# Optimization experiments

Measured on AMD Instinct MI355X. Metric: run time of the kernel, lower is better.

Reference implementation:

```python
import jax, jax.numpy as jnp
import numpy as np

B, LW, LE, D, H = 16, 512, 128, 1024, 16
DH = D // H  # 64
L = LW + LE


def _heads(x):
    # [B, L, D] -> [B, H, L, DH]
    b, l, _ = x.shape
    return x.reshape(b, l, H, DH).transpose(0, 2, 1, 3)


def setup_inputs() -> dict:
    key = jax.random.key(0)
    ks = jax.random.split(key, 20)
    s = 0.02
    def w(k):
        return jax.random.normal(k, (D, D), dtype=jnp.float32) * s
    def b(k):
        return jax.random.normal(k, (D,), dtype=jnp.float32) * s
    return {
        "word_hidden_states": jax.random.normal(ks[0], (B, LW, D), dtype=jnp.float32),
        "entity_hidden_states": jax.random.normal(ks[1], (B, LE, D), dtype=jnp.float32),
        "attention_mask": jnp.zeros((B, 1, 1, L), dtype=jnp.float32),
        "layer_num": 0,
        "qw": w(ks[2]), "qb": b(ks[3]),
        "kw": w(ks[4]), "kb": b(ks[5]),
        "vw": w(ks[6]), "vb": b(ks[7]),
        "w2e_qw": w(ks[8]), "w2e_qb": b(ks[9]),
        "w2e_kw": w(ks[10]), "w2e_kb": b(ks[11]),
        "e2w_qw": w(ks[12]), "e2w_qb": b(ks[13]),
        "e2w_kw": w(ks[14]), "e2w_kb": b(ks[15]),
    }


def reference(word_hidden_states, entity_hidden_states, attention_mask, layer_num,
              qw, qb, kw, kb, vw, vb,
              w2e_qw, w2e_qb, w2e_kw, w2e_kb,
              e2w_qw, e2w_qb, e2w_kw, e2w_kb):
    h = jnp.concatenate([word_hidden_states, entity_hidden_states], axis=1)  # [B,L,D]
    q = _heads(h @ qw + qb)
    k = _heads(h @ kw + kb)
    v = _heads(h @ vw + vb)
    scores = jnp.einsum("bhqd,bhkd->bhqk", q, k)  # [B,H,L,L]

    # cross-block gate scores
    w2e_q = _heads(word_hidden_states @ w2e_qw + w2e_qb)    # [B,H,LW,DH]
    w2e_k = _heads(entity_hidden_states @ w2e_kw + w2e_kb)  # [B,H,LE,DH]
    w2e = jnp.einsum("bhqd,bhkd->bhqk", w2e_q, w2e_k)       # [B,H,LW,LE]
    e2w_q = _heads(entity_hidden_states @ e2w_qw + e2w_qb)  # [B,H,LE,DH]
    e2w_k = _heads(word_hidden_states @ e2w_kw + e2w_kb)    # [B,H,LW,DH]
    e2w = jnp.einsum("bhqd,bhkd->bhqk", e2w_q, e2w_k)       # [B,H,LE,LW]

    # masked_scatter fills only cross blocks; elsewhere gate raw score is 0,
    # so sigmoid(0)*-10 = -5 on the word-word and entity-entity blocks.
    gate = jnp.full(scores.shape, -5.0, dtype=scores.dtype)
    gate = gate.at[:, :, :LW, LW:].set(jax.nn.sigmoid(w2e) * -10.0)
    gate = gate.at[:, :, LW:, :LW].set(jax.nn.sigmoid(e2w) * -10.0)

    scores = (scores + gate) / np.sqrt(DH).astype(np.float32)
    scores = scores + attention_mask
    probs = jax.nn.softmax(scores, axis=-1)
    ctx = jnp.einsum("bhqk,bhkd->bhqd", probs, v)  # [B,H,L,DH]
    ctx = ctx.transpose(0, 2, 1, 3).reshape(h.shape[0], L, D)
    return ctx[:, :LW, :], ctx[:, LW:, :]
```

## Files before the change

### kernel.cpp

```cpp
#include <hip/hip_runtime.h>
#include <hip/hip_bf16.h>
#include <stdint.h>

#define B_   16
#define LW_  512
#define LE_  128
#define L_   640
#define D_   1024
#define H_   16
#define DH_  64
#define M_   (B_*L_)
#define N_   (7*D_)
#define K_   D_

typedef __attribute__((ext_vector_type(8))) short short8;
typedef __attribute__((ext_vector_type(4))) float float4v;

__device__ __forceinline__ unsigned short f2bf(float x){
    union { float f; uint32_t u; } v; v.f = x;
    uint32_t u = v.u;
    return (unsigned short)((u + 0x7FFFu + ((u >> 16) & 1u)) >> 16);
}

__global__ __launch_bounds__(256) void prep_h(const float* __restrict__ word,
                                              const float* __restrict__ ent,
                                              unsigned short* __restrict__ hb){
    int idx = blockIdx.x*256 + threadIdx.x;
    int row = idx >> 7;
    int c   = (idx & 127) << 3;
    int b = row / L_, l = row - b*L_;
    const float* src = (l < LW_) ? (word + ((size_t)b*LW_ + l)*D_ + c)
                                 : (ent  + ((size_t)b*LE_ + (l-LW_))*D_ + c);
    float4 a0 = ((const float4*)src)[0];
    float4 a1 = ((const float4*)src)[1];
    uint4 o;
    o.x = f2bf(a0.x) | ((uint32_t)f2bf(a0.y)<<16);
    o.y = f2bf(a0.z) | ((uint32_t)f2bf(a0.w)<<16);
    o.z = f2bf(a1.x) | ((uint32_t)f2bf(a1.y)<<16);
    o.w = f2bf(a1.z) | ((uint32_t)f2bf(a1.w)<<16);
    *(uint4*)(hb + (size_t)row*D_ + c) = o;
}

__global__ __launch_bounds__(256) void prep_w(const float* __restrict__ w0, const float* __restrict__ w1,
                                              const float* __restrict__ w2, const float* __restrict__ w3,
                                              const float* __restrict__ w4, const float* __restrict__ w5,
                                              const float* __restrict__ w6,
                                              unsigned short* __restrict__ bt){
    __shared__ float t[64][65];
    int id = blockIdx.x;
    int kt = id & 15;
    int ntile = id >> 4;
    int p = ntile >> 4;
    int nin = (ntile & 15) * 64;
    const float* wp = (p==0)?w0:(p==1)?w1:(p==2)?w2:(p==3)?w3:(p==4)?w4:(p==5)?w5:w6;
    int k0 = kt*64;
    int tr  = threadIdx.x >> 4;
    int tc4 = (threadIdx.x & 15) * 4;
    for (int pass = 0; pass < 4; ++pass){
        int kl = pass*16 + tr;
        const float4 v = *(const float4*)(wp + (size_t)(k0+kl)*D_ + nin + tc4);
        t[kl][tc4+0]=v.x; t[kl][tc4+1]=v.y; t[kl][tc4+2]=v.z; t[kl][tc4+3]=v.w;
    }
    __syncthreads();
    for (int pass = 0; pass < 4; ++pass){
        int nl = pass*16 + tr;
        uint2 pk;
        pk.x = f2bf(t[tc4+0][nl]) | ((uint32_t)f2bf(t[tc4+1][nl])<<16);
        pk.y = f2bf(t[tc4+2][nl]) | ((uint32_t)f2bf(t[tc4+3][nl])<<16);
        *(uint2*)(bt + (size_t)(ntile*64 + nl)*K_ + k0 + tc4) = pk;
    }
}

__global__ __launch_bounds__(256) void prep_bias(const float* __restrict__ b0, const float* __restrict__ b1,
                                                 const float* __restrict__ b2, const float* __restrict__ b3,
                                                 const float* __restrict__ b4, const float* __restrict__ b5,
                                                 const float* __restrict__ b6,
                                                 float* __restrict__ biasAll){
    int n = blockIdx.x*256 + threadIdx.x;
    int p = n >> 10, c = n & 1023;
    const float* bp = (p==0)?b0:(p==1)?b1:(p==2)?b2:(p==3)?b3:(p==4)?b4:(p==5)?b5:b6;
    biasAll[n] = bp[c];
}

__global__ __launch_bounds__(256, 4) void gemm_proj(const unsigned short* __restrict__ hb,
                                                    const unsigned short* __restrict__ bt,
                                                    const float* __restrict__ biasAll,
                                                    unsigned short* __restrict__ C,
                                                    unsigned short* __restrict__ Vt){
    __shared__ unsigned short sA[128*64];
    __shared__ unsigned short sB[128*64];
    int tid = threadIdx.x;
    int wave = tid >> 6, lane = tid & 63;
    int quad = lane >> 4, l16 = lane & 15;
    int bm = blockIdx.x % 80, bn = blockIdx.x / 80;
    int m0 = bm*128, n0 = bn*128;
    int wm = wave >> 1, wn = wave & 1;
    float4v acc[4][4] = {};

    for (int kk = 0; kk < K_; kk += 64) {
        #pragma unroll
        for (int i = 0; i < 4; ++i) {
            int idx = i*256 + tid;
            int row = idx >> 3;
            int c8  = (((idx & 7) ^ (row & 7)) << 3);
            const unsigned short* ga = hb + (size_t)(m0 + row)*K_ + kk + c8;
            __builtin_amdgcn_global_load_lds(
                (const __attribute__((address_space(1))) void*)ga,
                (__attribute__((address_space(3))) void*)(sA + ((i*256 + wave*64) << 3)), 16, 0, 0);
            const unsigned short* gb = bt + (size_t)(n0 + row)*K_ + kk + c8;
            __builtin_amdgcn_global_load_lds(
                (const __attribute__((address_space(1))) void*)gb,
                (__attribute__((address_space(3))) void*)(sB + ((i*256 + wave*64) << 3)), 16, 0, 0);
        }
        __syncthreads();
        #pragma unroll
        for (int s = 0; s < 2; ++s) {
            short8 af[4], bf[4];
            #pragma unroll
            for (int i=0;i<4;i++){
                int row = wm*64 + i*16 + l16;
                af[i] = *(const short8*)(sA + (row << 6) + (((s*4 + quad) ^ (row & 7)) << 3));
            }
            #pragma unroll
            for (int j=0;j<4;j++){
                int row = wn*64 + j*16 + l16;
                bf[j] = *(const short8*)(sB + (row << 6) + (((s*4 + quad) ^ (row & 7)) << 3));
            }
            #pragma unroll
            for (int i=0;i<4;i++)
                #pragma unroll
                for (int j=0;j<4;j++)
                    acc[i][j] = __builtin_amdgcn_mfma_f32_16x16x32_bf16(af[i], bf[j], acc[i][j], 0,0,0);
        }
        __syncthreads();
    }

    bool isV = (n0 >= 2*D_) && (n0 < 3*D_);
    #pragma unroll
    for (int i=0;i<4;i++){
        int mrow = m0 + wm*64 + i*16 + quad*4;
        #pragma unroll
        for (int j=0;j<4;j++){
            int ncol = n0 + wn*64 + j*16 + l16;
            float bias = biasAll[ncol];
            if (!isV) {
                #pragma unroll
                for (int r=0;r<4;r++)
                    C[(size_t)(mrow + r)*N_ + ncol] = f2bf(acc[i][j][r] + bias);
            } else {
                int nv = ncol - 2*D_;
                int hh = nv >> 6, dd = nv & 63;
                int bb = mrow / L_, ll = mrow - bb*L_;
                uint2 pk;
                pk.x = f2bf(acc[i][j][0]+bias) | ((uint32_t)f2bf(acc[i][j][1]+bias)<<16);
                pk.y = f2bf(acc[i][j][2]+bias) | ((uint32_t)f2bf(acc[i][j][3]+bias)<<16);
                *(uint2*)(Vt + ((size_t)(bb*H_ + hh)*DH_ + dd)*L_ + ll) = pk;
            }
        }
    }
}


__device__ __forceinline__ void tile_ld(const unsigned short* __restrict__ g, size_t stride,
                                        unsigned short* lds, int wave, int lane){
    #pragma unroll
    for (int p = 0; p < 2; ++p){
        int c = p*256 + wave*64 + lane;
        int r = c >> 3, js = c & 7;
        const unsigned short* ga = g + (size_t)r*stride + ((js ^ (r & 7)) << 3);
        __builtin_amdgcn_global_load_lds(
            (const __attribute__((address_space(1))) void*)ga,
            (__attribute__((address_space(3))) void*)(lds + ((p*256 + wave*64) << 3)), 16, 0, 0);
    }
}

__device__ __forceinline__ short8 frag64(const unsigned short* lds, int row, int jj){
    return *(const short8*)(lds + (row << 6) + (((jj ^ (row & 7)) << 3)));
}

__global__ __launch_bounds__(256, 2) void attn(const unsigned short* __restrict__ C,
                                               const unsigned short* __restrict__ Vt,
                                               const float* __restrict__ mask,
                                               float* __restrict__ out){
    int id = blockIdx.x;
    int qt = id % 5; id /= 5;
    int h  = id % H_; int b = id / H_;
    bool isWord = (qt < 4);
    int tid = threadIdx.x, wave = tid>>6, lane = tid&63, quad = lane>>4, l16 = lane&15;

    __shared__ unsigned short sK0 [64*64];
    __shared__ unsigned short sK1 [64*64];
    __shared__ unsigned short sGK0[64*64];
    __shared__ unsigned short sGK1[64*64];
    __shared__ unsigned short sV0 [64*64];
    __shared__ unsigned short sV1 [64*64];
    __shared__ unsigned short sP  [64*64];
    __shared__ float sMask[L_];

    const unsigned short* Kg  = C  + (size_t)(b*L_)*N_ + D_ + h*DH_;
    const unsigned short* GKg = C  + (size_t)(b*L_)*N_ + (isWord?4:6)*D_ + h*DH_;
    const unsigned short* Vg  = Vt + ((size_t)(b*H_ + h)*DH_)*L_;

    tile_ld(Kg, N_, sK0, wave, lane);
    tile_ld(Vg, L_, sV0, wave, lane);
    if (!isWord) tile_ld(GKg, N_, sGK0, wave, lane);

    for (int i = tid; i < L_; i += 256) sMask[i] = mask[b*L_ + i];

    int qrowbase = b*L_ + qt*128 + wave*32;
    short8 qf[2][2], gqf[2][2];
    #pragma unroll
    for (int mi=0; mi<2; ++mi){
        const unsigned short* qb_ = C + (size_t)(qrowbase + mi*16 + l16)*N_ + h*DH_;
        const unsigned short* gq_ = C + (size_t)(qrowbase + mi*16 + l16)*N_ + (isWord?3:5)*D_ + h*DH_;
        qf[mi][0]  = *(const short8*)(qb_ + quad*8);
        qf[mi][1]  = *(const short8*)(qb_ + 32 + quad*8);
        gqf[mi][0] = *(const short8*)(gq_ + quad*8);
        gqf[mi][1] = *(const short8*)(gq_ + 32 + quad*8);
    }

    float4v O[2][4] = {};
    float lrow[2][4] = {};

    __syncthreads();

    auto step = [&](int kt,
                    unsigned short* sKc, unsigned short* sGKc, unsigned short* sVc,
                    unsigned short* sKn, unsigned short* sGKn, unsigned short* sVn){
        if (kt < 9) {
            tile_ld(Kg + (size_t)((kt+1)*64)*N_, N_, sKn, wave, lane);
            tile_ld(Vg + (kt+1)*64, L_, sVn, wave, lane);
            bool g1 = isWord ? (kt+1 >= 8) : (kt+1 < 8);
            if (g1) tile_ld(GKg + (size_t)((kt+1)*64)*N_, N_, sGKn, wave, lane);
        }
        bool gated = isWord ? (kt >= 8) : (kt < 8);

        float4v S[2][4];
        #pragma unroll
        for (int nt=0; nt<4; ++nt){
            short8 k0 = frag64(sKc, nt*16 + l16, quad);
            short8 k1 = frag64(sKc, nt*16 + l16, 4 + quad);
            #pragma unroll
            for (int mi=0; mi<2; ++mi){
                float4v s = {};
                s = __builtin_amdgcn_mfma_f32_16x16x32_bf16(qf[mi][0], k0, s, 0,0,0);
                s = __builtin_amdgcn_mfma_f32_16x16x32_bf16(qf[mi][1], k1, s, 0,0,0);
                S[mi][nt] = s;
            }
        }
        if (gated) {
            #pragma unroll
            for (int nt=0; nt<4; ++nt){
                short8 g0 = frag64(sGKc, nt*16 + l16, quad);
                short8 g1 = frag64(sGKc, nt*16 + l16, 4 + quad);
                #pragma unroll
                for (int mi=0; mi<2; ++mi){
                    float4v g = {};
                    g = __builtin_amdgcn_mfma_f32_16x16x32_bf16(gqf[mi][0], g0, g, 0,0,0);
                    g = __builtin_amdgcn_mfma_f32_16x16x32_bf16(gqf[mi][1], g1, g, 0,0,0);
                    #pragma unroll
                    for (int r=0;r<4;r++){
                        float sig = 1.f/(1.f + __expf(-g[r]));
                        S[mi][nt][r] = 0.125f*S[mi][nt][r] - 1.25f*sig;
                    }
                }
            }
        } else {
            #pragma unroll
            for (int mi=0;mi<2;mi++)
                #pragma unroll
                for (int nt=0;nt<4;nt++)
                    #pragma unroll
                    for (int r=0;r<4;r++) S[mi][nt][r] = 0.125f*S[mi][nt][r] - 0.625f;
        }
        #pragma unroll
        for (int mi=0;mi<2;mi++){
            #pragma unroll
            for (int nt=0;nt<4;nt++){
                float mv = sMask[kt*64 + nt*16 + l16];
                #pragma unroll
                for (int r=0;r<4;r++){
                    float p = __expf(S[mi][nt][r] + mv);
                    S[mi][nt][r] = p;
                    lrow[mi][r] += p;
                }
            }
            #pragma unroll
            for (int nt=0;nt<4;nt++)
                #pragma unroll
                for (int r=0;r<4;r++){
                    int row = wave*16 + quad*4 + r;
                    int col = nt*16 + l16;
                    int j = col >> 3, jo = col & 7;
                    sP[(row<<6) + (((j ^ (row & 7))<<3) | jo)] = f2bf(S[mi][nt][r]);
                }
            #pragma unroll
            for (int ks=0; ks<2; ++ks){
                short8 pf = frag64(sP, wave*16 + l16, ks*4 + quad);
                #pragma unroll
                for (int nt=0;nt<4;nt++){
                    short8 vf = frag64(sVc, nt*16 + l16, ks*4 + quad);
                    O[mi][nt] = __builtin_amdgcn_mfma_f32_16x16x32_bf16(pf, vf, O[mi][nt], 0,0,0);
                }
            }
        }
        __syncthreads();
    };

    for (int k2 = 0; k2 < 10; k2 += 2){
        step(k2,   sK0, sGK0, sV0, sK1, sGK1, sV1);
        step(k2+1, sK1, sGK1, sV1, sK0, sGK0, sV0);
    }

    #pragma unroll
    for (int mi=0;mi<2;mi++)
        #pragma unroll
        for (int r=0;r<4;r++){
            float s = lrow[mi][r];
            #pragma unroll
            for (int off=1; off<16; off<<=1) s += __shfl_xor(s, off, 64);
            lrow[mi][r] = 1.f/s;
        }

    #pragma unroll
    for (int mi=0;mi<2;mi++){
        int q0 = qt*128 + wave*32 + mi*16 + quad*4;
        #pragma unroll
        for (int nt=0;nt<4;nt++){
            int d = h*DH_ + nt*16 + l16;
            #pragma unroll
            for (int r=0;r<4;r++){
                int q = q0 + r;
                float v = O[mi][nt][r]*lrow[mi][r];
                size_t off;
                if (q < LW_) off = ((size_t)(b*LW_ + q))*D_ + d;
                else         off = (size_t)B_*LW_*D_ + ((size_t)(b*LE_ + (q-LW_)))*D_ + d;
                out[off] = v;
            }
        }
    }
}

extern "C" void kernel_launch(void* const* d_in, const int* in_sizes, int n_in,
                              void* d_out, int out_size, void* d_ws, size_t ws_size,
                              hipStream_t stream)
{
    const float* word  = (const float*)d_in[0];
    const float* ent   = (const float*)d_in[1];
    const float* mask  = (const float*)d_in[2];
    const float* qw    = (const float*)d_in[4];  const float* qb_   = (const float*)d_in[5];
    const float* kw    = (const float*)d_in[6];  const float* kb_   = (const float*)d_in[7];
    const float* vw    = (const float*)d_in[8];  const float* vb_   = (const float*)d_in[9];
    const float* w2eqw = (const float*)d_in[10]; const float* w2eqb = (const float*)d_in[11];
    const float* w2ekw = (const float*)d_in[12]; const float* w2ekb = (const float*)d_in[13];
    const float* e2wqw = (const float*)d_in[14]; const float* e2wqb = (const float*)d_in[15];
    const float* e2wkw = (const float*)d_in[16]; const float* e2wkb = (const float*)d_in[17];

    char* ws = (char*)d_ws;
    unsigned short* hb      = (unsigned short*)(ws);
    unsigned short* bt      = (unsigned short*)(ws + 20971520);
    float*          biasAll = (float*)        (ws + 35651584);
    unsigned short* C       = (unsigned short*)(ws + 35680256);
    unsigned short* Vt      = (unsigned short*)(ws + 182480896);

    prep_h   <<<5120, 256, 0, stream>>>(word, ent, hb);
    prep_w   <<<1792, 256, 0, stream>>>(qw, kw, vw, w2eqw, w2ekw, e2wqw, e2wkw, bt);
    prep_bias<<<28,   256, 0, stream>>>(qb_, kb_, vb_, w2eqb, w2ekb, e2wqb, e2wkb, biasAll);
    gemm_proj<<<4480, 256, 0, stream>>>(hb, bt, biasAll, C, Vt);
    attn     <<<1280, 256, 0, stream>>>(C, Vt, mask, (float*)d_out);
}
```

Measured before the change: 373.2 us.

## Skip unused gate projection tiles, fuse bias prep, load V from global

```diff
diff --git a/kernel.cpp b/kernel.cpp
--- a/kernel.cpp
+++ b/kernel.cpp
@@ -24,7 +24,19 @@
 
 __global__ __launch_bounds__(256) void prep_h(const float* __restrict__ word,
                                               const float* __restrict__ ent,
-                                              unsigned short* __restrict__ hb){
+                                              unsigned short* __restrict__ hb,
+                                              const float* __restrict__ b0, const float* __restrict__ b1,
+                                              const float* __restrict__ b2, const float* __restrict__ b3,
+                                              const float* __restrict__ b4, const float* __restrict__ b5,
+                                              const float* __restrict__ b6,
+                                              float* __restrict__ biasAll){
+    if (blockIdx.x >= 5120) {
+        int n = (blockIdx.x - 5120)*256 + threadIdx.x;
+        int p = n >> 10, c = n & 1023;
+        const float* bp = (p==0)?b0:(p==1)?b1:(p==2)?b2:(p==3)?b3:(p==4)?b4:(p==5)?b5:b6;
+        biasAll[n] = bp[c];
+        return;
+    }
     int idx = blockIdx.x*256 + threadIdx.x;
     int row = idx >> 7;
     int c   = (idx & 127) << 3;
@@ -71,17 +83,6 @@
     }
 }
 
-__global__ __launch_bounds__(256) void prep_bias(const float* __restrict__ b0, const float* __restrict__ b1,
-                                                 const float* __restrict__ b2, const float* __restrict__ b3,
-                                                 const float* __restrict__ b4, const float* __restrict__ b5,
-                                                 const float* __restrict__ b6,
-                                                 float* __restrict__ biasAll){
-    int n = blockIdx.x*256 + threadIdx.x;
-    int p = n >> 10, c = n & 1023;
-    const float* bp = (p==0)?b0:(p==1)?b1:(p==2)?b2:(p==3)?b3:(p==4)?b4:(p==5)?b5:b6;
-    biasAll[n] = bp[c];
-}
-
 __global__ __launch_bounds__(256, 4) void gemm_proj(const unsigned short* __restrict__ hb,
                                                     const unsigned short* __restrict__ bt,
                                                     const float* __restrict__ biasAll,
@@ -92,8 +93,19 @@
     int tid = threadIdx.x;
     int wave = tid >> 6, lane = tid & 63;
     int quad = lane >> 4, l16 = lane & 15;
-    int bm = blockIdx.x % 80, bn = blockIdx.x / 80;
-    int m0 = bm*128, n0 = bn*128;
+
+    int bid = blockIdx.x;
+    int m0, n0;
+    if (bid < 1920) { int bm = bid % 80, bn = bid / 80; m0 = bm*128; n0 = bn*128; }
+    else {
+        int g = bid - 1920;
+        if (g < 512)      { int mt = g & 63; m0 = (mt>>2)*640 + (mt&3)*128; n0 = 3072 + (g>>6)*128; }
+        else if (g < 640) { int e = g-512;   m0 = (e&15)*640 + 512;         n0 = 4096 + (e>>4)*128; }
+        else if (g < 768) { int e = g-640;   m0 = (e&15)*640 + 512;         n0 = 5120 + (e>>4)*128; }
+        else              { int e = g-768; int mt = e & 63;
+                            m0 = (mt>>2)*640 + (mt&3)*128;                  n0 = 6144 + (e>>6)*128; }
+    }
+
     int wm = wave >> 1, wn = wave & 1;
     float4v acc[4][4] = {};
 
@@ -178,7 +190,7 @@
     return *(const short8*)(lds + (row << 6) + (((jj ^ (row & 7)) << 3)));
 }
 
-__global__ __launch_bounds__(256, 2) void attn(const unsigned short* __restrict__ C,
+__global__ __launch_bounds__(256, 3) void attn(const unsigned short* __restrict__ C,
                                                const unsigned short* __restrict__ Vt,
                                                const float* __restrict__ mask,
                                                float* __restrict__ out){
@@ -192,8 +204,6 @@
     __shared__ unsigned short sK1 [64*64];
     __shared__ unsigned short sGK0[64*64];
     __shared__ unsigned short sGK1[64*64];
-    __shared__ unsigned short sV0 [64*64];
-    __shared__ unsigned short sV1 [64*64];
     __shared__ unsigned short sP  [64*64];
     __shared__ float sMask[L_];
 
@@ -202,7 +212,6 @@
     const unsigned short* Vg  = Vt + ((size_t)(b*H_ + h)*DH_)*L_;
 
     tile_ld(Kg, N_, sK0, wave, lane);
-    tile_ld(Vg, L_, sV0, wave, lane);
     if (!isWord) tile_ld(GKg, N_, sGK0, wave, lane);
 
     for (int i = tid; i < L_; i += 256) sMask[i] = mask[b*L_ + i];
@@ -225,11 +234,10 @@
     __syncthreads();
 
     auto step = [&](int kt,
-                    unsigned short* sKc, unsigned short* sGKc, unsigned short* sVc,
-                    unsigned short* sKn, unsigned short* sGKn, unsigned short* sVn){
+                    unsigned short* sKc, unsigned short* sGKc,
+                    unsigned short* sKn, unsigned short* sGKn){
         if (kt < 9) {
             tile_ld(Kg + (size_t)((kt+1)*64)*N_, N_, sKn, wave, lane);
-            tile_ld(Vg + (kt+1)*64, L_, sVn, wave, lane);
             bool g1 = isWord ? (kt+1 >= 8) : (kt+1 < 8);
             if (g1) tile_ld(GKg + (size_t)((kt+1)*64)*N_, N_, sGKn, wave, lane);
         }
@@ -248,6 +256,13 @@
                 S[mi][nt] = s;
             }
         }
+        short8 vf[2][4];
+        #pragma unroll
+        for (int ks=0; ks<2; ++ks)
+            #pragma unroll
+            for (int nt=0;nt<4;nt++)
+                vf[ks][nt] = *(const short8*)(Vg + (size_t)(nt*16 + l16)*L_ + kt*64 + ks*32 + quad*8);
+
         if (gated) {
             #pragma unroll
             for (int nt=0; nt<4; ++nt){
@@ -298,18 +313,16 @@
             for (int ks=0; ks<2; ++ks){
                 short8 pf = frag64(sP, wave*16 + l16, ks*4 + quad);
                 #pragma unroll
-                for (int nt=0;nt<4;nt++){
-                    short8 vf = frag64(sVc, nt*16 + l16, ks*4 + quad);
-                    O[mi][nt] = __builtin_amdgcn_mfma_f32_16x16x32_bf16(pf, vf, O[mi][nt], 0,0,0);
-                }
+                for (int nt=0;nt<4;nt++)
+                    O[mi][nt] = __builtin_amdgcn_mfma_f32_16x16x32_bf16(pf, vf[ks][nt], O[mi][nt], 0,0,0);
             }
         }
         __syncthreads();
     };
 
     for (int k2 = 0; k2 < 10; k2 += 2){
-        step(k2,   sK0, sGK0, sV0, sK1, sGK1, sV1);
-        step(k2+1, sK1, sGK1, sV1, sK0, sGK0, sV0);
+        step(k2,   sK0, sGK0, sK1, sGK1);
+        step(k2+1, sK1, sGK1, sK0, sGK0);
     }
 
     #pragma unroll
@@ -363,9 +376,9 @@
     unsigned short* C       = (unsigned short*)(ws + 35680256);
     unsigned short* Vt      = (unsigned short*)(ws + 182480896);
 
-    prep_h   <<<5120, 256, 0, stream>>>(word, ent, hb);
+    prep_h   <<<5148, 256, 0, stream>>>(word, ent, hb,
+                                        qb_, kb_, vb_, w2eqb, w2ekb, e2wqb, e2wkb, biasAll);
     prep_w   <<<1792, 256, 0, stream>>>(qw, kw, vw, w2eqw, w2ekw, e2wqw, e2wkw, bt);
-    prep_bias<<<28,   256, 0, stream>>>(qb_, kb_, vb_, w2eqb, w2ekb, e2wqb, e2wkb, biasAll);
-    gemm_proj<<<4480, 256, 0, stream>>>(hb, bt, biasAll, C, Vt);
+    gemm_proj<<<3200, 256, 0, stream>>>(hb, bt, biasAll, C, Vt);
     attn     <<<1280, 256, 0, stream>>>(C, Vt, mask, (float*)d_out);
 }
```

Result: slower. 487.3 us (+30.6%).
